# Optimization experiments

Hardware: AMD Instinct MI355X
Metric: run time of the kernel (lower is better)

Reference implementation:

```python
import jax, jax.numpy as jnp
from jax import lax
import numpy as np

DN = ('NCHW', 'OIHW', 'NCHW')

def _leaky(x):
    return jnp.where(x > 0, x, 0.2 * x)

def _forward(texts, styles, conv1_w, conv1_b, conv2_w, conv2_b, proj_w, proj_b,
             v1_w, v1_b, v2_w, v2_b, v3_w, v3_b, d1_w, d1_b, d2_w, d2_b):
    bs, tot, W, H = texts.shape
    C = proj_w.shape[1]  # style_channels
    # stack text/style as 2-channel images: [bs*tot, 2, W, H]
    ts = jnp.stack((texts, styles), axis=2).reshape(bs * tot, 2, W, H)
    # transnet: conv -> leaky -> conv -> leaky -> GAP -> linear
    x = lax.conv_general_dilated(ts, conv1_w, (2, 2), 'SAME', dimension_numbers=DN)
    x = _leaky(x + conv1_b[None, :, None, None])
    x = lax.conv_general_dilated(x, conv2_w, (2, 2), 'SAME', dimension_numbers=DN)
    x = _leaky(x + conv2_b[None, :, None, None])
    x = x.mean(axis=(2, 3))                              # [bs*tot, 64]
    feats = (x @ proj_w + proj_b).reshape(bs, tot, C)     # [bs, tot, C]
    # vec2vec scorer MLP -> tanh score per option
    h = _leaky(feats @ v1_w + v1_b)
    h = _leaky(h @ v2_w + v2_b)
    score = jnp.tanh(h @ v3_w + v3_b)[..., 0]             # [bs, tot]
    # top-1 routing: argmax + gather of the selected style vector
    idx = jnp.argmax(score, axis=1)                       # [bs]
    res = jnp.take_along_axis(feats, idx[:, None, None], axis=1)[:, 0]  # [bs, C]
    # vec2im decoder: MLP -> image [bs, 1, W, H]
    img = jnp.tanh(_leaky(res @ d1_w + d1_b) @ d2_w + d2_b)
    return img.reshape(bs, 1, W, H)

def setup_inputs() -> dict:
    key = jax.random.key(0)
    ks = jax.random.split(key, 12)
    bs, tot, W, H = 32, 64, 64, 64
    C, C1, C2, NFC, DH = 128, 32, 64, 128, 512
    s = 0.05
    def rn(k, shape):
        return jax.random.normal(k, shape, dtype=jnp.float32) * s
    return {
        'texts': jax.random.normal(ks[0], (bs, tot, W, H), dtype=jnp.float32),
        'styles': jax.random.normal(ks[1], (bs, tot, W, H), dtype=jnp.float32),
        'conv1_w': rn(ks[2], (C1, 2, 3, 3)),
        'conv1_b': jnp.zeros((C1,), jnp.float32),
        'conv2_w': rn(ks[3], (C2, C1, 3, 3)),
        'conv2_b': jnp.zeros((C2,), jnp.float32),
        'proj_w': rn(ks[4], (C2, C)),
        'proj_b': jnp.zeros((C,), jnp.float32),
        'v1_w': rn(ks[5], (C, NFC)),
        'v1_b': jnp.zeros((NFC,), jnp.float32),
        'v2_w': rn(ks[6], (NFC, NFC)),
        'v2_b': jnp.zeros((NFC,), jnp.float32),
        'v3_w': rn(ks[7], (NFC, 1)),
        'v3_b': jnp.zeros((1,), jnp.float32),
        'd1_w': rn(ks[8], (C, DH)),
        'd1_b': jnp.zeros((DH,), jnp.float32),
        'd2_w': rn(ks[9], (DH, W * H)),
        'd2_b': jnp.zeros((W * H,), jnp.float32),
    }

def reference(texts, styles, conv1_w, conv1_b, conv2_w, conv2_b, proj_w, proj_b,
              v1_w, v1_b, v2_w, v2_b, v3_w, v3_b, d1_w, d1_b, d2_w, d2_b):
    return _forward(texts, styles, conv1_w, conv1_b, conv2_w, conv2_b, proj_w, proj_b,
                    v1_w, v1_b, v2_w, v2_b, v3_w, v3_b, d1_w, d1_b, d2_w, d2_b)
```

## Files before the change

### kernel.cpp

```cpp
#include <hip/hip_runtime.h>
#include <cstddef>
#include <cstdint>

#define LEAKY(x) ((x) > 0.f ? (x) : 0.2f*(x))

typedef _Float16 f16x8  __attribute__((ext_vector_type(8)));
typedef float    f32x4  __attribute__((ext_vector_type(4)));
typedef float    f32x16 __attribute__((ext_vector_type(16)));

#define WS_FEATS   0
#define WS_SCORES  262144
#define WS_W2      268288
#define WS_W1M     287744
#define WS_GAPP    288768

__global__ void kPack(const float* __restrict__ c1w, const float* __restrict__ c2w,
                      float* __restrict__ ws)
{
    _Float16* W2 = (_Float16*)(ws + WS_W2);
    _Float16* W1 = (_Float16*)(ws + WS_W1M);
    const int t = blockIdx.x*256 + threadIdx.x;
    for (int i = t; i < 2*2*9*2*64*8; i += 64*256) {
        int idx = i;
        const int e   = idx & 7;  idx >>= 3;
        const int co  = idx & 63; idx >>= 6;
        const int hf  = idx & 1;  idx >>= 1;
        const int tap = idx % 9;  idx /= 9;
        const int pl  = idx & 1;
        const int ck  = idx >> 1;
        const int cil = hf*8 + e;
        float wv = c2w[(co*32 + ck*16 + cil)*9 + tap];
        _Float16 h = (_Float16)wv;
        W2[i] = pl ? (_Float16)(wv - (float)h) : h;
    }
    if (t < 2048) {
        int pl = t >> 10, rest = t & 1023;
        int co = rest >> 5, k = rest & 31;
        int kh = k >> 3, j = k & 7, kw = j >> 1, ci = j & 1;
        float wv = 0.f;
        if (kh < 3 && kw < 3) wv = c1w[co*18 + ci*9 + kh*3 + kw];
        _Float16 hi = (_Float16)wv;
        W1[t] = pl ? (_Float16)(wv - (float)hi) : hi;
    }
}

__device__ __forceinline__ int x1_off(int pl, int hf, int row, int xp, int xq) {
    return (pl*2 + hf)*2528 + row*280 + (xp*17 + xq)*8;
}
#define X1_HALFS (2*2*2528)

__global__ __launch_bounds__(512) void kConv(
    const float* __restrict__ texts, const float* __restrict__ styles,
    const float* __restrict__ c1b, const float* __restrict__ c2b,
    const float* __restrict__ wsro, float* __restrict__ gapp)
{
    __shared__ __align__(16) union {
        _Float16 in[2][19][68][2];
        float    part[4][32];
    } s_u;
    __shared__ __align__(16) _Float16 s_x1[2][X1_HALFS];

    const int bid = blockIdx.x, tid = threadIdx.x;
    const int n = bid >> 2, q = bid & 3;
    const int w = tid >> 6, l = tid & 63;

    {
        const uint4 z4 = {0u,0u,0u,0u};
        uint4* z = (uint4*)&s_x1[0][0];
        for (int i = tid; i < 2*X1_HALFS/8; i += 512) z[i] = z4;
        if (tid < 38) {
            int pl = tid >= 19, row = pl ? tid - 19 : tid;
            *(uint4*)&s_u.in[pl][row][64][0] = z4;
        }
    }
    for (int u = tid; u < 304; u += 512) {
        const int row = u >> 4, g = u & 15;
        const int grow = q*16 + row;
        float4 tv = {0.f,0.f,0.f,0.f}, sv = {0.f,0.f,0.f,0.f};
        if (grow < 64) {
            tv = *(const float4*)&texts [(size_t)n*4096 + grow*64 + g*4];
            sv = *(const float4*)&styles[(size_t)n*4096 + grow*64 + g*4];
        }
        float vals[8] = {tv.x, sv.x, tv.y, sv.y, tv.z, sv.z, tv.w, sv.w};
        _Float16 hh[8], ll[8];
        #pragma unroll
        for (int j = 0; j < 8; ++j) {
            _Float16 hi = (_Float16)vals[j];
            hh[j] = hi; ll[j] = (_Float16)(vals[j] - (float)hi);
        }
        *(uint4*)&s_u.in[0][row][g*4][0] = *(uint4*)hh;
        *(uint4*)&s_u.in[1][row][g*4][0] = *(uint4*)ll;
    }
    __syncthreads();

    const _Float16* W2h = (const _Float16*)(wsro + WS_W2);
    const _Float16* W1g = (const _Float16*)(wsro + WS_W1M);

    f32x16 acc;
    #pragma unroll
    for (int r = 0; r < 16; ++r) acc[r] = 0.f;

    const int ck = w >> 2, sw = w & 3;
    const int mt = (w >> 1) & 1, nh = w & 1;
    const int posl = mt*32 + (l & 31);
    const int py2 = posl >> 4, px2 = posl & 15;
    const int hf2 = l >> 5;
    const int co2 = nh*32 + (l & 31);
    const int kg = l >> 4, m16 = l & 15;
    const int NT = (q == 3) ? 16 : 18;

    {
        f16x8 a_h = *(const f16x8*)&W1g[(0*32 + ck*16 + m16)*32 + kg*8];
        f16x8 a_l = *(const f16x8*)&W1g[(1*32 + ck*16 + m16)*32 + kg*8];
        float4 b4 = *(const float4*)&c1b[ck*16 + kg*4];
        for (int t = sw; t < NT; t += 4) {
            const int py = t >> 1, px = (t & 1)*16 + m16;
            const int row = (kg < 3) ? (2*py + kg) : (2*py);
            const _Float16* bp0 = &s_u.in[0][row][2*px][0];
            const _Float16* bp1 = &s_u.in[1][row][2*px][0];
            f16x8 b_h, b_l;
            ((uint2*)&b_h)[0] = *(const uint2*)bp0;
            ((uint2*)&b_h)[1] = *(const uint2*)(bp0 + 4);
            ((uint2*)&b_l)[0] = *(const uint2*)bp1;
            ((uint2*)&b_l)[1] = *(const uint2*)(bp1 + 4);
            f32x4 c = {0.f,0.f,0.f,0.f};
            c = __builtin_amdgcn_mfma_f32_16x16x32_f16(a_l, b_h, c, 0, 0, 0);
            c = __builtin_amdgcn_mfma_f32_16x16x32_f16(a_h, b_l, c, 0, 0, 0);
            c = __builtin_amdgcn_mfma_f32_16x16x32_f16(a_h, b_h, c, 0, 0, 0);
            const int xp = px & 1, xq = px >> 1;
            _Float16 hh[4], ll[4];
            #pragma unroll
            for (int r = 0; r < 4; ++r) {
                float v = c[r] + b4[r];
                v = fmaxf(v, 0.2f*v);
                _Float16 hi = (_Float16)v;
                hh[r] = hi; ll[r] = (_Float16)(v - (float)hi);
            }
            const int eo = (kg & 1)*4;
            *(uint2*)&s_x1[ck][x1_off(0, kg >> 1, py, xp, xq) + eo] = *(uint2*)hh;
            *(uint2*)&s_x1[ck][x1_off(1, kg >> 1, py, xp, xq) + eo] = *(uint2*)ll;
        }
    }
    __syncthreads();

    {
        const _Float16* Bg_h = W2h + (size_t)(ck*2 + 0)*9216 + hf2*512 + co2*8;
        const _Float16* Bg_l = Bg_h + 9216;
        #pragma unroll
        for (int tap = 0; tap < 9; ++tap) {
            const int kh = tap/3, kw = tap%3;
            const int xr = 2*px2 + kw;
            const int xp = xr & 1, xq = xr >> 1;
            const int r2 = 2*py2 + kh;
            f16x8 Ah = *(const f16x8*)&s_x1[ck][x1_off(0, hf2, r2, xp, xq)];
            f16x8 Al = *(const f16x8*)&s_x1[ck][x1_off(1, hf2, r2, xp, xq)];
            f16x8 Bh = *(const f16x8*)&Bg_h[tap*1024];
            f16x8 Bl = *(const f16x8*)&Bg_l[tap*1024];
            acc = __builtin_amdgcn_mfma_f32_32x32x16_f16(Ah, Bh, acc, 0, 0, 0);
            acc = __builtin_amdgcn_mfma_f32_32x32x16_f16(Al, Bh, acc, 0, 0, 0);
            acc = __builtin_amdgcn_mfma_f32_32x32x16_f16(Ah, Bl, acc, 0, 0, 0);
        }
    }
    __syncthreads();

    float* comb = (float*)&s_x1[0][0];
    if (ck == 1) {
        float* dst = comb + ((w - 4)*64 + l)*18;
        #pragma unroll
        for (int r = 0; r < 16; r += 2)
            *(float2*)&dst[r] = make_float2(acc[r], acc[r+1]);
    }
    __syncthreads();
    if (ck == 0) {
        const float* src = comb + (w*64 + l)*18;
        const float b2 = c2b[co2];
        float s = 0.f;
        #pragma unroll
        for (int r = 0; r < 16; ++r) {
            float v = acc[r] + src[r] + b2;
            s += fmaxf(v, 0.2f*v);
        }
        s += __shfl_xor(s, 32);
        if (l < 32) s_u.part[w][l] = s;
    }
    __syncthreads();
    if (tid < 64) {
        const int nhc = tid >> 5, cl = tid & 31;
        float g = s_u.part[0*2 + nhc][cl] + s_u.part[1*2 + nhc][cl];
        gapp[(size_t)(n*4 + q)*64 + tid] = g;
    }
}

__global__ __launch_bounds__(128) void kScore(
    const float* __restrict__ gapp,
    const float* __restrict__ pw,  const float* __restrict__ pb,
    const float* __restrict__ v1w, const float* __restrict__ v1b,
    const float* __restrict__ v2w, const float* __restrict__ v2b,
    const float* __restrict__ v3w, const float* __restrict__ v3b,
    float* __restrict__ feats, float* __restrict__ scores)
{
    __shared__ float s_gap[64], s_f[128], s_h[128], s_red[2];
    const int n = blockIdx.x, tid = threadIdx.x;

    if (tid < 64) {
        const float* gp = &gapp[(size_t)n*256 + tid];
        s_gap[tid] = (gp[0] + gp[64] + gp[128] + gp[192]) * (1.f/256.f);
    }
    __syncthreads();
    {
        float a = pb[tid];
        #pragma unroll 8
        for (int m = 0; m < 64; ++m) a += s_gap[m]*pw[m*128 + tid];
        feats[(size_t)n*128 + tid] = a;
        s_f[tid] = a;
    }
    __syncthreads();
    {
        float a = v1b[tid];
        #pragma unroll 8
        for (int m = 0; m < 128; ++m) a += s_f[m]*v1w[m*128 + tid];
        s_h[tid] = LEAKY(a);
    }
    __syncthreads();
    {
        float a = v2b[tid];
        #pragma unroll 8
        for (int m = 0; m < 128; ++m) a += s_h[m]*v2w[m*128 + tid];
        a = LEAKY(a);
        s_f[tid] = a * v3w[tid];
    }
    __syncthreads();
    {
        float p = s_f[tid];
        #pragma unroll
        for (int off = 32; off; off >>= 1) p += __shfl_xor(p, off);
        if ((tid & 63) == 0) s_red[tid >> 6] = p;
    }
    __syncthreads();
    if (tid == 0) scores[n] = tanhf(s_red[0] + s_red[1] + v3b[0]);
}

__global__ __launch_bounds__(512) void kDecode(
    const float* __restrict__ scores, const float* __restrict__ feats,
    const float* __restrict__ d1w, const float* __restrict__ d1b,
    const float* __restrict__ d2w, const float* __restrict__ d2b,
    float* __restrict__ out)
{
    __shared__ float s_res[128];
    __shared__ float s_h[512];
    __shared__ int s_idx;
    const int bid = blockIdx.x;
    const int b = bid >> 3, ot = bid & 7;
    const int tid = threadIdx.x;

    if (tid < 64) {
        float v = scores[b*64 + tid];
        int   i = tid;
        #pragma unroll
        for (int off = 32; off; off >>= 1) {
            float ov = __shfl_xor(v, off);
            int   oi = __shfl_xor(i, off);
            if (ov > v || (ov == v && oi < i)) { v = ov; i = oi; }
        }
        if (tid == 0) s_idx = i;
    }
    __syncthreads();
    if (tid < 128) s_res[tid] = feats[((size_t)b*64 + s_idx)*128 + tid];
    __syncthreads();
    {
        float a = d1b[tid];
        #pragma unroll 8
        for (int m = 0; m < 128; ++m) a += s_res[m]*d1w[m*512 + tid];
        s_h[tid] = LEAKY(a);
    }
    __syncthreads();
    const int o = ot*512 + tid;
    float a = d2b[o];
    for (int k = 0; k < 512; k += 4) {
        float4 h4 = *(const float4*)&s_h[k];
        a += h4.x*d2w[(size_t)(k+0)*4096 + o];
        a += h4.y*d2w[(size_t)(k+1)*4096 + o];
        a += h4.z*d2w[(size_t)(k+2)*4096 + o];
        a += h4.w*d2w[(size_t)(k+3)*4096 + o];
    }
    out[(size_t)b*4096 + o] = tanhf(a);
}

extern "C" void kernel_launch(void* const* d_in, const int* in_sizes, int n_in,
                              void* d_out, int out_size, void* d_ws, size_t ws_size,
                              hipStream_t stream)
{
    const float* texts  = (const float*)d_in[0];
    const float* styles = (const float*)d_in[1];
    const float* c1w = (const float*)d_in[2];
    const float* c1b = (const float*)d_in[3];
    const float* c2w = (const float*)d_in[4];
    const float* c2b = (const float*)d_in[5];
    const float* pw  = (const float*)d_in[6];
    const float* pb  = (const float*)d_in[7];
    const float* v1w = (const float*)d_in[8];
    const float* v1b = (const float*)d_in[9];
    const float* v2w = (const float*)d_in[10];
    const float* v2b = (const float*)d_in[11];
    const float* v3w = (const float*)d_in[12];
    const float* v3b = (const float*)d_in[13];
    const float* d1w = (const float*)d_in[14];
    const float* d1b = (const float*)d_in[15];
    const float* d2w = (const float*)d_in[16];
    const float* d2b = (const float*)d_in[17];

    float* ws     = (float*)d_ws;
    float* feats  = ws + WS_FEATS;
    float* scores = ws + WS_SCORES;
    float* gapp   = ws + WS_GAPP;

    kPack<<<dim3(64), dim3(256), 0, stream>>>(c1w, c2w, ws);
    kConv<<<dim3(8192), dim3(512), 0, stream>>>(
        texts, styles, c1b, c2b, (const float*)ws, gapp);
    kScore<<<dim3(2048), dim3(128), 0, stream>>>(
        gapp, pw, pb, v1w, v1b, v2w, v2b, v3w, v3b, feats, scores);
    kDecode<<<dim3(256), dim3(512), 0, stream>>>(
        scores, feats, d1w, d1b, d2w, d2b, (float*)d_out);
}
```

Before: 125.6 us.

## Batch multiple samples per block in score and decode MLPs, trim conv smem zeroing

kScore now processes 8 samples per block and kDecode 4 batch rows per block. Each weight load is reused across several accumulators, which cuts global weight traffic by 8x and 4x. kConv no longer zeroes the whole x1 staging buffer and clears only the halo/pad regions, with an extra region cleared for the last quarter tile. The trade-off is far fewer blocks (256 and 64), so the MLP stages have less parallelism on a large GPU, and the selective zeroing depends on correctly covering every padded location.

```diff
diff --git a/kernel.cpp b/kernel.cpp
--- a/kernel.cpp
+++ b/kernel.cpp
@@ -66,8 +66,19 @@
 
     {
         const uint4 z4 = {0u,0u,0u,0u};
-        uint4* z = (uint4*)&s_x1[0][0];
-        for (int i = tid; i < 2*X1_HALFS/8; i += 512) z[i] = z4;
+        if (tid < 72) {
+            int i = tid;
+            const int ck = i >= 36; i -= ck*36;
+            const int pl = i >= 18; i -= pl*18;
+            const int hf = i >= 9;  const int row = i - hf*9;
+            *(uint4*)&s_x1[ck][x1_off(pl, hf, row, 0, 16)] = z4;
+        }
+        if (q == 3 && tid >= 128 && tid < 400) {
+            const int i = tid - 128;
+            const int grp = i / 34, s = i - grp*34;
+            const int ck = grp >> 2, pl = (grp >> 1) & 1, hf = grp & 1;
+            *(uint4*)&s_x1[ck][(pl*2 + hf)*2528 + 8*280 + s*8] = z4;
+        }
         if (tid < 38) {
             int pl = tid >= 19, row = pl ? tid - 19 : tid;
             *(uint4*)&s_u.in[pl][row][64][0] = z4;
@@ -199,45 +210,67 @@
     const float* __restrict__ v3w, const float* __restrict__ v3b,
     float* __restrict__ feats, float* __restrict__ scores)
 {
-    __shared__ float s_gap[64], s_f[128], s_h[128], s_red[2];
-    const int n = blockIdx.x, tid = threadIdx.x;
-
-    if (tid < 64) {
-        const float* gp = &gapp[(size_t)n*256 + tid];
-        s_gap[tid] = (gp[0] + gp[64] + gp[128] + gp[192]) * (1.f/256.f);
-    }
-    __syncthreads();
-    {
-        float a = pb[tid];
-        #pragma unroll 8
-        for (int m = 0; m < 64; ++m) a += s_gap[m]*pw[m*128 + tid];
-        feats[(size_t)n*128 + tid] = a;
-        s_f[tid] = a;
-    }
-    __syncthreads();
-    {
-        float a = v1b[tid];
-        #pragma unroll 8
-        for (int m = 0; m < 128; ++m) a += s_f[m]*v1w[m*128 + tid];
-        s_h[tid] = LEAKY(a);
-    }
-    __syncthreads();
-    {
-        float a = v2b[tid];
-        #pragma unroll 8
-        for (int m = 0; m < 128; ++m) a += s_h[m]*v2w[m*128 + tid];
-        a = LEAKY(a);
-        s_f[tid] = a * v3w[tid];
-    }
-    __syncthreads();
-    {
-        float p = s_f[tid];
-        #pragma unroll
-        for (int off = 32; off; off >>= 1) p += __shfl_xor(p, off);
-        if ((tid & 63) == 0) s_red[tid >> 6] = p;
-    }
-    __syncthreads();
-    if (tid == 0) scores[n] = tanhf(s_red[0] + s_red[1] + v3b[0]);
+    __shared__ float s_gap[8][64], s_f[8][128], s_h[8][128], s_red[8][2];
+    const int n0 = blockIdx.x*8, tid = threadIdx.x;
+
+    for (int i = tid; i < 512; i += 128) {
+        const int g = i >> 6, c = i & 63;
+        const float* gp = &gapp[(size_t)(n0 + g)*256 + c];
+        s_gap[g][c] = (gp[0] + gp[64] + gp[128] + gp[192]) * (1.f/256.f);
+    }
+    __syncthreads();
+    {
+        float a[8];
+        const float b = pb[tid];
+        #pragma unroll
+        for (int g = 0; g < 8; ++g) a[g] = b;
+        for (int m = 0; m < 64; ++m) {
+            const float wv = pw[m*128 + tid];
+            #pragma unroll
+            for (int g = 0; g < 8; ++g) a[g] += s_gap[g][m]*wv;
+        }
+        #pragma unroll
+        for (int g = 0; g < 8; ++g) {
+            feats[(size_t)(n0 + g)*128 + tid] = a[g];
+            s_f[g][tid] = a[g];
+        }
+    }
+    __syncthreads();
+    {
+        float a[8];
+        const float b = v1b[tid];
+        #pragma unroll
+        for (int g = 0; g < 8; ++g) a[g] = b;
+        for (int m = 0; m < 128; ++m) {
+            const float wv = v1w[m*128 + tid];
+            #pragma unroll
+            for (int g = 0; g < 8; ++g) a[g] += s_f[g][m]*wv;
+        }
+        #pragma unroll
+        for (int g = 0; g < 8; ++g) s_h[g][tid] = LEAKY(a[g]);
+    }
+    __syncthreads();
+    {
+        float a[8];
+        const float b = v2b[tid];
+        #pragma unroll
+        for (int g = 0; g < 8; ++g) a[g] = b;
+        for (int m = 0; m < 128; ++m) {
+            const float wv = v2w[m*128 + tid];
+            #pragma unroll
+            for (int g = 0; g < 8; ++g) a[g] += s_h[g][m]*wv;
+        }
+        const float v3 = v3w[tid];
+        #pragma unroll
+        for (int g = 0; g < 8; ++g) {
+            float p = LEAKY(a[g]) * v3;
+            #pragma unroll
+            for (int off = 32; off; off >>= 1) p += __shfl_xor(p, off);
+            if ((tid & 63) == 0) s_red[g][tid >> 6] = p;
+        }
+    }
+    __syncthreads();
+    if (tid < 8) scores[n0 + tid] = tanhf(s_red[tid][0] + s_red[tid][1] + v3b[0]);
 }
 
 __global__ __launch_bounds__(512) void kDecode(
@@ -246,44 +279,61 @@
     const float* __restrict__ d2w, const float* __restrict__ d2b,
     float* __restrict__ out)
 {
-    __shared__ float s_res[128];
-    __shared__ float s_h[512];
-    __shared__ int s_idx;
+    __shared__ float s_res[4][128];
+    __shared__ float s_h[4][512];
+    __shared__ int s_idx[4];
     const int bid = blockIdx.x;
-    const int b = bid >> 3, ot = bid & 7;
+    const int bg = bid >> 3, ot = bid & 7;
+    const int b0 = bg*4;
     const int tid = threadIdx.x;
 
-    if (tid < 64) {
-        float v = scores[b*64 + tid];
-        int   i = tid;
+    if (tid < 256) {
+        const int g = tid >> 6, lane = tid & 63;
+        float v = scores[(b0 + g)*64 + lane];
+        int   i = lane;
         #pragma unroll
         for (int off = 32; off; off >>= 1) {
             float ov = __shfl_xor(v, off);
             int   oi = __shfl_xor(i, off);
             if (ov > v || (ov == v && oi < i)) { v = ov; i = oi; }
         }
-        if (tid == 0) s_idx = i;
-    }
-    __syncthreads();
-    if (tid < 128) s_res[tid] = feats[((size_t)b*64 + s_idx)*128 + tid];
-    __syncthreads();
-    {
-        float a = d1b[tid];
-        #pragma unroll 8
-        for (int m = 0; m < 128; ++m) a += s_res[m]*d1w[m*512 + tid];
-        s_h[tid] = LEAKY(a);
+        if (lane == 0) s_idx[g] = i;
+    }
+    __syncthreads();
+    if (tid < 512) {
+        const int g = tid >> 7, j = tid & 127;
+        if (g < 4) s_res[g][j] = feats[((size_t)(b0 + g)*64 + s_idx[g])*128 + j];
+    }
+    __syncthreads();
+    {
+        float a[4];
+        const float b = d1b[tid];
+        #pragma unroll
+        for (int g = 0; g < 4; ++g) a[g] = b;
+        for (int m = 0; m < 128; ++m) {
+            const float wv = d1w[m*512 + tid];
+            #pragma unroll
+            for (int g = 0; g < 4; ++g) a[g] += s_res[g][m]*wv;
+        }
+        #pragma unroll
+        for (int g = 0; g < 4; ++g) s_h[g][tid] = LEAKY(a[g]);
     }
     __syncthreads();
     const int o = ot*512 + tid;
-    float a = d2b[o];
-    for (int k = 0; k < 512; k += 4) {
-        float4 h4 = *(const float4*)&s_h[k];
-        a += h4.x*d2w[(size_t)(k+0)*4096 + o];
-        a += h4.y*d2w[(size_t)(k+1)*4096 + o];
-        a += h4.z*d2w[(size_t)(k+2)*4096 + o];
-        a += h4.w*d2w[(size_t)(k+3)*4096 + o];
-    }
-    out[(size_t)b*4096 + o] = tanhf(a);
+    float a[4];
+    {
+        const float b = d2b[o];
+        #pragma unroll
+        for (int g = 0; g < 4; ++g) a[g] = b;
+    }
+    for (int k = 0; k < 512; ++k) {
+        const float wv = d2w[(size_t)k*4096 + o];
+        #pragma unroll
+        for (int g = 0; g < 4; ++g) a[g] += s_h[g][k]*wv;
+    }
+    #pragma unroll
+    for (int g = 0; g < 4; ++g)
+        out[(size_t)(b0 + g)*4096 + o] = tanhf(a[g]);
 }
 
 extern "C" void kernel_launch(void* const* d_in, const int* in_sizes, int n_in,
@@ -317,8 +367,8 @@
     kPack<<<dim3(64), dim3(256), 0, stream>>>(c1w, c2w, ws);
     kConv<<<dim3(8192), dim3(512), 0, stream>>>(
         texts, styles, c1b, c2b, (const float*)ws, gapp);
-    kScore<<<dim3(2048), dim3(128), 0, stream>>>(
+    kScore<<<dim3(256), dim3(128), 0, stream>>>(
         gapp, pw, pb, v1w, v1b, v2w, v2b, v3w, v3b, feats, scores);
-    kDecode<<<dim3(256), dim3(512), 0, stream>>>(
+    kDecode<<<dim3(64), dim3(512), 0, stream>>>(
         scores, feats, d1w, d1b, d2w, d2b, (float*)d_out);
 }
```

Result: slower. 148.1 us (+17.9%).
